# Optimization experiments

Hardware: AMD Instinct MI355X
Metric: run time of the kernel (lower is better)

Reference implementation:

```python
import jax, jax.numpy as jnp
import numpy as np

N_NODES = 10000
N_EDGES = 320000
IN_FEATS = 500
CONV_DIMS = [500, 256, 256]
FC_DIMS = [256, 128, 40]
BN_EPS = 1e-5


def setup_inputs() -> dict:
    key = jax.random.key(0)
    ks = jax.random.split(key, 16)
    inp = {
        "x": jax.random.normal(ks[0], (N_NODES, IN_FEATS), dtype=jnp.float32),
        "edge_index": jax.random.randint(ks[1], (2, N_EDGES), 0, N_NODES, dtype=jnp.int64),
    }
    # conv layer params: Linear W [in,out], b [out]; BatchNorm gamma/beta [out]
    ki = 2
    for li in range(len(CONV_DIMS) - 1):
        d_in, d_out = CONV_DIMS[li], CONV_DIMS[li + 1]
        s = 1.0 / np.sqrt(d_in)
        inp[f"conv_W{li}"] = jax.random.uniform(ks[ki], (d_in, d_out), jnp.float32, -s, s); ki += 1
        inp[f"conv_b{li}"] = jax.random.uniform(ks[ki], (d_out,), jnp.float32, -s, s); ki += 1
        inp[f"bn_g{li}"] = jnp.ones((d_out,), jnp.float32)
        inp[f"bn_b{li}"] = jnp.zeros((d_out,), jnp.float32)
    for li in range(len(FC_DIMS) - 1):
        d_in, d_out = FC_DIMS[li], FC_DIMS[li + 1]
        s = 1.0 / np.sqrt(d_in)
        inp[f"fc_W{li}"] = jax.random.uniform(ks[ki], (d_in, d_out), jnp.float32, -s, s); ki += 1
        inp[f"fc_b{li}"] = jax.random.uniform(ks[ki], (d_out,), jnp.float32, -s, s); ki += 1
    return inp


def _degree(edge_index, n, dtype):
    # Faithful to: A = eye(N); A[i,j] = 1 per edge (set semantics dedupes repeats).
    A = jnp.eye(n, dtype=dtype).at[edge_index[0], edge_index[1]].set(1.0)
    return A.sum(axis=1)  # deg_i = rowsum of A


def _batchnorm(h, g, b):
    # training-mode BatchNorm1d: batch stats, biased variance
    mean = h.mean(axis=0)
    var = h.var(axis=0)
    return (h - mean) * jax.lax.rsqrt(var + BN_EPS) * g + b


def reference(x, edge_index, conv_W0, conv_b0, bn_g0, bn_b0,
              conv_W1, conv_b1, bn_g1, bn_b1,
              fc_W0, fc_b0, fc_W1, fc_b1):
    n = x.shape[0]
    deg = _degree(edge_index, n, x.dtype)
    # D = sqrt(diag(deg)) is a diagonal matrix, so elementwise D*A*D = diag(deg);
    # mm(D*A*D, x) == deg[:, None] * x (exactly the original math).
    h = x
    for W, b, g, beta in ((conv_W0, conv_b0, bn_g0, bn_b0),
                          (conv_W1, conv_b1, bn_g1, bn_b1)):
        h = (deg[:, None] * h) @ W + b
        h = jax.nn.relu(h)
        h = _batchnorm(h, g, beta)
        # dropout: identity at inference
    for W, b in ((fc_W0, fc_b0), (fc_W1, fc_b1)):
        h = jax.nn.relu(h @ W + b)  # original appends ReLU after every fc, incl. last
    return h
```

## Files before the change

kernel.cpp:

```cpp
#include <hip/hip_runtime.h>

#define NN 10000
#define NE 320000
#define MP 10112
#define BN_EPS 1e-5f

#define NRANGE 64
#define BROWS 160
#define NBUCK 128
#define HBITS 5120
#define HWORDS 160
#define BCAP  4096
#define EPB   5000

typedef __attribute__((ext_vector_type(8))) short short8;
typedef __attribute__((ext_vector_type(4))) float f32x4;
typedef unsigned short u16;

__device__ __forceinline__ void split1(float v, u16& h, u16& l) {
    unsigned int u = __float_as_uint(v);
    h = (u16)(u >> 16);
    float hf = __uint_as_float(u & 0xFFFF0000u);
    l = (u16)(__float_as_uint(v - hf) >> 16);
}

__device__ __forceinline__ void gll16(const void* g, void* l) {
    __builtin_amdgcn_global_load_lds(
        (const __attribute__((address_space(1))) unsigned int*)g,
        (__attribute__((address_space(3))) unsigned int*)l, 16, 0, 0);
}

__device__ void splitW_dev(const float* __restrict__ W, int K, int N, int Kp, int Np,
                           u16* __restrict__ Wt, int bx, int by, char* smem) {
    float (*tile)[65] = (float(*)[65])smem;
    int t = threadIdx.x;
    int bk = bx * 64, bn = by * 64;
    #pragma unroll
    for (int p = 0; p < 4; ++p) {
        int kk = (t >> 4) + p * 16;
        int nc = (t & 15) * 4;
        int k = bk + kk;
        float4 v = {0.f, 0.f, 0.f, 0.f};
        if (k < K && bn + nc + 3 < N)
            v = *(const float4*)&W[(size_t)k * N + bn + nc];
        tile[kk][nc] = v.x; tile[kk][nc + 1] = v.y;
        tile[kk][nc + 2] = v.z; tile[kk][nc + 3] = v.w;
    }
    __syncthreads();
    int nn = t >> 2;
    int kk0 = (t & 3) * 16;
    u16 hs[16], ls[16];
    #pragma unroll
    for (int j = 0; j < 16; ++j) split1(tile[kk0 + j][nn], hs[j], ls[j]);
    size_t ob = (size_t)(bn + nn) * Kp + bk + kk0;
    size_t lo = (size_t)Np * Kp;
    *(short8*)&Wt[ob] = *(short8*)hs;
    *(short8*)&Wt[ob + 8] = *(short8*)&hs[8];
    *(short8*)&Wt[lo + ob] = *(short8*)ls;
    *(short8*)&Wt[lo + ob + 8] = *(short8*)&ls[8];
}

__device__ void xsplit_dev(const float* __restrict__ x, u16* __restrict__ xs, int gblk) {
    int t = threadIdx.x;
    int r0 = gblk * 16 + (t >> 4);
    int l = t & 15;
    u16* xlo = xs + (size_t)MP * 512;
    #pragma unroll
    for (int j = 0; j < 8; ++j) {
        int k = (l + j * 16) * 4;
        float vals[4] = {0.f, 0.f, 0.f, 0.f};
        if (r0 < NN && k < 500) {
            float4 v = *(const float4*)&x[(size_t)r0 * 500 + k];
            vals[0] = v.x; vals[1] = v.y; vals[2] = v.z; vals[3] = v.w;
        }
        ushort4 hs, ls;
        split1(vals[0], hs.x, ls.x); split1(vals[1], hs.y, ls.y);
        split1(vals[2], hs.z, ls.z); split1(vals[3], hs.w, ls.w);
        *(ushort4*)&xs[(size_t)r0 * 512 + k] = hs;
        *(ushort4*)&xlo[(size_t)r0 * 512 + k] = ls;
    }
}

__global__ __launch_bounds__(256)
void scatter_prep(const int* __restrict__ ei,
                  unsigned* __restrict__ bucketArr, unsigned* __restrict__ gcount,
                  const float* __restrict__ x,
                  const float* __restrict__ W0, const float* __restrict__ fW1,
                  u16* __restrict__ xs, u16* __restrict__ W0t, u16* __restrict__ fW1t) {
    __shared__ char smem[16704];
    __shared__ unsigned cnt[NBUCK], basep[NBUCK];
    int b = blockIdx.x;
    int t = threadIdx.x;
    if (b < 64) {
        if (t < NBUCK) cnt[t] = 0;
        __syncthreads();
        int base = b * EPB;
        unsigned myb[20], myk[20];
        #pragma unroll
        for (int k = 0; k < 20; ++k) {
            int el = t + k * 256;
            myb[k] = 0xFFFFFFFFu;
            if (el < EPB) {
                int e = base + el;
                unsigned i = (unsigned)ei[e], j = (unsigned)ei[NE + e];
                unsigned bk = (i / BROWS) * 2 + (j >= HBITS ? 1u : 0u);
                myb[k] = bk;
                myk[k] = (i << 14) | j;
                atomicAdd(&cnt[bk], 1u);
            }
        }
        __syncthreads();
        if (t < NBUCK) { basep[t] = atomicAdd(&gcount[t * 16], cnt[t]); cnt[t] = 0; }
        __syncthreads();
        #pragma unroll
        for (int k = 0; k < 20; ++k) {
            if (myb[k] != 0xFFFFFFFFu) {
                unsigned bk = myb[k];
                unsigned pos = basep[bk] + atomicAdd(&cnt[bk], 1u);
                if (pos < BCAP) bucketArr[(size_t)bk * BCAP + pos] = myk[k];
            }
        }
    } else if (b < 696) {
        xsplit_dev(x, xs, b - 64);
    } else if (b < 728) {
        int idx = b - 696;
        splitW_dev(W0, 500, 256, 512, 256, W0t, idx & 7, idx >> 3, smem);
    } else {
        splitW_dev(fW1, 128, 40, 128, 64, fW1t, b - 728, 0, smem);
    }
}

__global__ __launch_bounds__(256)
void bucket_degree(const unsigned* __restrict__ bucketArr,
                   const unsigned* __restrict__ gcount,
                   float* __restrict__ deg) {
    __shared__ unsigned lbm[BROWS * HWORDS];
    int b = blockIdx.x, t = threadIdx.x;
    int rr = b >> 1, h = b & 1;
    int row0 = rr * BROWS;
    {
        uint4* z = (uint4*)lbm;
        #pragma unroll
        for (int i = 0; i < 25; ++i) z[t + i * 256] = (uint4){0u, 0u, 0u, 0u};
    }
    __syncthreads();
    for (int r = t; r < BROWS; r += 256) {
        int i = row0 + r;
        if (i < NN && ((i >= HBITS) == (h == 1))) {
            int jj = i - h * HBITS;
            atomicOr(&lbm[r * HWORDS + (jj >> 5)], 1u << (jj & 31));
        }
    }
    unsigned n = gcount[b * 16];
    const unsigned* keys = bucketArr + (size_t)b * BCAP;
    for (unsigned k = t; k < n; k += 256) {
        unsigned key = keys[k];
        unsigned i = key >> 14, j = key & 0x3FFFu;
        unsigned r = i - row0;
        unsigned jj = j - h * HBITS;
        atomicOr(&lbm[r * HWORDS + (jj >> 5)], 1u << (jj & 31));
    }
    __syncthreads();
    #pragma unroll
    for (int pass = 0; pass < 3; ++pass) {
        int r = pass * 64 + (t >> 2), wl = t & 3;
        if (r >= BROWS) break;
        int i = row0 + r;
        int c = 0;
        const uint4* rp = (const uint4*)&lbm[r * HWORDS + wl * 40];
        #pragma unroll
        for (int m = 0; m < 10; ++m) {
            uint4 v = rp[m];
            c += __popc(v.x) + __popc(v.y) + __popc(v.z) + __popc(v.w);
        }
        c += __shfl_down(c, 1, 4);
        c += __shfl_down(c, 2, 4);
        if (wl == 0 && i < NN) atomicAdd(&deg[i], (float)c);
    }
}

__global__ __launch_bounds__(256, 4)
void conv0_gemm(const u16* __restrict__ Ahi, const u16* __restrict__ Alo,
                const u16* __restrict__ Bhi, const u16* __restrict__ Blo,
                const float* __restrict__ deg, const float* __restrict__ bias,
                float* __restrict__ stats,
                u16* __restrict__ Ohi, u16* __restrict__ Olo) {
    __shared__ char smem[32768];
    __shared__ float sdeg[64];
    const int Kp = 512, M = NN, No = 256;
    const int b = blockIdx.x;
    const int xcd = b & 7, g = b >> 3;
    const int bx = g & 3, by = (g >> 2) * 8 + xcd;
    if (by >= 158) return;
    const int t = threadIdx.x;
    const int lane = t & 63;
    const int w = t >> 6;
    const int q = lane >> 4;
    const int l16 = lane & 15;
    const int m7 = l16 & 7;
    const int row0 = by * 64;
    const int col0 = bx * 64;

    const u16* bases[4] = {Ahi, Alo, Bhi, Blo};
    const u16* srcs[8];
    unsigned dstoff[8];
    #pragma unroll
    for (int i = 0; i < 8; ++i) {
        int gi = w + i * 4;
        int reg = i >> 1;
        int j = gi & 7;
        int rb = (reg < 2) ? row0 : col0;
        int r = j * 8 + (lane >> 3);
        int c = (lane & 7) ^ (r & 7);
        srcs[i] = bases[reg] + (size_t)(rb + r) * Kp + c * 8;
        dstoff[i] = reg * 8192 + j * 1024;
    }

    f32x4 acc[4];
    #pragma unroll
    for (int s = 0; s < 4; ++s) acc[s] = (f32x4){0.f, 0.f, 0.f, 0.f};

    #pragma unroll
    for (int i = 0; i < 8; ++i) { gll16(srcs[i], smem + dstoff[i]); srcs[i] += 64; }

    if (t < 64) sdeg[t] = deg[row0 + t];

    for (int k0 = 0; k0 < Kp; k0 += 64) {
        __syncthreads();
        short8 ah[2], al[2], bh[2][4], bl[2][4];
        #pragma unroll
        for (int kc = 0; kc < 2; ++kc) {
            int aoff = (w * 16 + l16) * 128 + (((kc * 4 + q) ^ m7) * 16);
            ah[kc] = *(const short8*)(smem + aoff);
            al[kc] = *(const short8*)(smem + 8192 + aoff);
            #pragma unroll
            for (int s = 0; s < 4; ++s) {
                int boff = (s * 16 + l16) * 128 + (((kc * 4 + q) ^ m7) * 16);
                bh[kc][s] = *(const short8*)(smem + 16384 + boff);
                bl[kc][s] = *(const short8*)(smem + 24576 + boff);
            }
        }
        __syncthreads();
        if (k0 + 64 < Kp) {
            #pragma unroll
            for (int i = 0; i < 8; ++i) { gll16(srcs[i], smem + dstoff[i]); srcs[i] += 64; }
        }
        #pragma unroll
        for (int kc = 0; kc < 2; ++kc)
            #pragma unroll
            for (int s = 0; s < 4; ++s) {
                acc[s] = __builtin_amdgcn_mfma_f32_16x16x32_bf16(al[kc], bh[kc][s], acc[s], 0, 0, 0);
                acc[s] = __builtin_amdgcn_mfma_f32_16x16x32_bf16(ah[kc], bl[kc][s], acc[s], 0, 0, 0);
                acc[s] = __builtin_amdgcn_mfma_f32_16x16x32_bf16(ah[kc], bh[kc][s], acc[s], 0, 0, 0);
            }
    }

    int growb = row0 + w * 16 + q * 4;
    float dgv[4];
    #pragma unroll
    for (int r = 0; r < 4; ++r) {
        int grow = growb + r;
        dgv[r] = (grow < M) ? sdeg[grow - row0] : 0.f;
    }
    #pragma unroll
    for (int s = 0; s < 4; ++s) {
        int gc = col0 + s * 16 + l16;
        float bia = bias[gc];
        float s_sum = 0.f, ss_sum = 0.f;
        #pragma unroll
        for (int r = 0; r < 4; ++r) {
            int grow = growb + r;
            bool real = grow < M;
            float v = fmaxf(fmaf(dgv[r], acc[s][r], bia), 0.f);
            if (!real) v = 0.f;
            s_sum += v; ss_sum += v * v;
            float vo = v * dgv[r];
            u16 h, l; split1(vo, h, l);
            Ohi[(size_t)grow * No + gc] = h;
            Olo[(size_t)grow * No + gc] = l;
        }
        s_sum  += __shfl_xor(s_sum, 16);  s_sum  += __shfl_xor(s_sum, 32);
        ss_sum += __shfl_xor(ss_sum, 16); ss_sum += __shfl_xor(ss_sum, 32);
        if (lane < 16) {
            atomicAdd(&stats[gc], s_sum);
            atomicAdd(&stats[256 + gc], ss_sum);
        }
    }
}

__global__ __launch_bounds__(256, 4)
void conv1_fold(const u16* __restrict__ Ahi, const u16* __restrict__ Alo,
                const float* __restrict__ W1, const float* __restrict__ stats0,
                const float* __restrict__ g0, const float* __restrict__ bb0,
                const float* __restrict__ b1, const float* __restrict__ deg,
                float* __restrict__ stats1, u16* __restrict__ Ohi, u16* __restrict__ Olo) {
    __shared__ char smem[32768];
    __shared__ float scl[256], sh[256], cred[256], cvec[64];
    const int Kp = 256, M = NN, No = 256;
    const int b = blockIdx.x;
    const int xcd = b & 7, g = b >> 3;
    const int bx = g & 3, by = (g >> 2) * 8 + xcd;
    if (by >= 158) return;
    const int t = threadIdx.x;
    const int lane = t & 63;
    const int w = t >> 6;
    const int q = lane >> 4;
    const int l16 = lane & 15;
    const int m7 = l16 & 7;
    const int row0 = by * 64;
    const int col0 = bx * 64;

    const u16* srcs[4];
    unsigned dstoff[4];
    #pragma unroll
    for (int i = 0; i < 4; ++i) {
        int gi = w + i * 4;
        int plane = gi >> 3, j = gi & 7;
        int r = j * 8 + (lane >> 3);
        int c = (lane & 7) ^ (r & 7);
        srcs[i] = (plane ? Alo : Ahi) + (size_t)(row0 + r) * Kp + c * 8;
        dstoff[i] = plane * 8192 + j * 1024;
    }
    #pragma unroll
    for (int i = 0; i < 4; ++i) { gll16(srcs[i], smem + dstoff[i]); srcs[i] += 64; }

    {
        float mean = stats0[t] * (1.f / NN);
        float var = stats0[256 + t] * (1.f / NN) - mean * mean;
        float s = g0[t] * rsqrtf(var + BN_EPS);
        scl[t] = s;
        sh[t] = bb0[t] - mean * s;
    }
    __syncthreads();
    {
        float s = 0.f;
        int n = col0 + (t & 63);
        #pragma unroll 8
        for (int k = (t >> 6); k < 256; k += 4)
            s += sh[k] * W1[(size_t)k * 256 + n];
        cred[t] = s;
        __syncthreads();
        if (t < 64) cvec[t] = cred[t] + cred[t + 64] + cred[t + 128] + cred[t + 192];
    }
    const int bn = t & 63;
    const int kb = (t >> 6) * 16;
    const int ch0 = (t >> 6) * 2;
    float vals[16];
    {
        const float* wp = W1 + (size_t)kb * 256 + col0 + bn;
        #pragma unroll
        for (int i = 0; i < 16; ++i) vals[i] = wp[(size_t)i * 256] * scl[kb + i];
    }

    f32x4 acc[4];
    #pragma unroll
    for (int s = 0; s < 4; ++s) acc[s] = (f32x4){0.f, 0.f, 0.f, 0.f};

    for (int k0 = 0; k0 < Kp; k0 += 64) {
        {
            u16 hs[16], ls[16];
            #pragma unroll
            for (int i = 0; i < 16; ++i) split1(vals[i], hs[i], ls[i]);
            unsigned o0 = bn * 128 + ((ch0 ^ (bn & 7)) * 16);
            unsigned o1 = bn * 128 + (((ch0 + 1) ^ (bn & 7)) * 16);
            *(short8*)(smem + 16384 + o0) = *(short8*)&hs[0];
            *(short8*)(smem + 16384 + o1) = *(short8*)&hs[8];
            *(short8*)(smem + 24576 + o0) = *(short8*)&ls[0];
            *(short8*)(smem + 24576 + o1) = *(short8*)&ls[8];
        }
        __syncthreads();
        short8 ah[2], al[2], bh[2][4], bl[2][4];
        #pragma unroll
        for (int kc = 0; kc < 2; ++kc) {
            int aoff = (w * 16 + l16) * 128 + (((kc * 4 + q) ^ m7) * 16);
            ah[kc] = *(const short8*)(smem + aoff);
            al[kc] = *(const short8*)(smem + 8192 + aoff);
            #pragma unroll
            for (int s = 0; s < 4; ++s) {
                int boff = (s * 16 + l16) * 128 + (((kc * 4 + q) ^ m7) * 16);
                bh[kc][s] = *(const short8*)(smem + 16384 + boff);
                bl[kc][s] = *(const short8*)(smem + 24576 + boff);
            }
        }
        __syncthreads();
        if (k0 + 64 < Kp) {
            #pragma unroll
            for (int i = 0; i < 4; ++i) { gll16(srcs[i], smem + dstoff[i]); srcs[i] += 64; }
            const float* wp = W1 + (size_t)(k0 + 64 + kb) * 256 + col0 + bn;
            #pragma unroll
            for (int i = 0; i < 16; ++i) vals[i] = wp[(size_t)i * 256] * scl[k0 + 64 + kb + i];
        }
        #pragma unroll
        for (int kc = 0; kc < 2; ++kc)
            #pragma unroll
            for (int s = 0; s < 4; ++s) {
                acc[s] = __builtin_amdgcn_mfma_f32_16x16x32_bf16(al[kc], bh[kc][s], acc[s], 0, 0, 0);
                acc[s] = __builtin_amdgcn_mfma_f32_16x16x32_bf16(ah[kc], bl[kc][s], acc[s], 0, 0, 0);
                acc[s] = __builtin_amdgcn_mfma_f32_16x16x32_bf16(ah[kc], bh[kc][s], acc[s], 0, 0, 0);
            }
    }

    int growb = row0 + w * 16 + q * 4;
    float dgv[4];
    #pragma unroll
    for (int r = 0; r < 4; ++r) dgv[r] = (growb + r < M) ? deg[growb + r] : 0.f;
    #pragma unroll
    for (int s = 0; s < 4; ++s) {
        int gc = col0 + s * 16 + l16;
        float bia = b1[gc];
        float cv = cvec[s * 16 + l16];
        float s_sum = 0.f, ss_sum = 0.f;
        #pragma unroll
        for (int r = 0; r < 4; ++r) {
            int grow = growb + r;
            bool real = grow < M;
            float v = fmaxf(fmaf(dgv[r], cv, acc[s][r] + bia), 0.f);
            if (!real) v = 0.f;
            s_sum += v; ss_sum += v * v;
            u16 h, l; split1(v, h, l);
            Ohi[(size_t)grow * No + gc] = h;
            Olo[(size_t)grow * No + gc] = l;
        }
        s_sum  += __shfl_xor(s_sum, 16);  s_sum  += __shfl_xor(s_sum, 32);
        ss_sum += __shfl_xor(ss_sum, 16); ss_sum += __shfl_xor(ss_sum, 32);
        if (lane < 16) {
            atomicAdd(&stats1[gc], s_sum);
            atomicAdd(&stats1[256 + gc], ss_sum);
        }
    }
}

__global__ __launch_bounds__(256, 4)
void fc0_fold(const u16* __restrict__ Ahi, const u16* __restrict__ Alo,
              const float* __restrict__ fW0, const float* __restrict__ stats1,
              const float* __restrict__ g1, const float* __restrict__ bb1,
              const float* __restrict__ fb0,
              u16* __restrict__ Ohi, u16* __restrict__ Olo) {
    __shared__ char smem[32768];
    __shared__ float scl[256], sh[256], cred[256], biasf[64];
    const int Kp = 256, M = NN, No = 128;
    const int b = blockIdx.x;
    const int xcd = b & 7, g = b >> 3;
    const int bx = g & 1, by = (g >> 1) * 8 + xcd;
    if (by >= 158) return;
    const int t = threadIdx.x;
    const int lane = t & 63;
    const int w = t >> 6;
    const int q = lane >> 4;
    const int l16 = lane & 15;
    const int m7 = l16 & 7;
    const int row0 = by * 64;
    const int col0 = bx * 64;

    const u16* srcs[4];
    unsigned dstoff[4];
    #pragma unroll
    for (int i = 0; i < 4; ++i) {
        int gi = w + i * 4;
        int plane = gi >> 3, j = gi & 7;
        int r = j * 8 + (lane >> 3);
        int c = (lane & 7) ^ (r & 7);
        srcs[i] = (plane ? Alo : Ahi) + (size_t)(row0 + r) * Kp + c * 8;
        dstoff[i] = plane * 8192 + j * 1024;
    }
    #pragma unroll
    for (int i = 0; i < 4; ++i) { gll16(srcs[i], smem + dstoff[i]); srcs[i] += 64; }

    {
        float mean = stats1[t] * (1.f / NN);
        float var = stats1[256 + t] * (1.f / NN) - mean * mean;
        float s = g1[t] * rsqrtf(var + BN_EPS);
        scl[t] = s;
        sh[t] = bb1[t] - mean * s;
    }
    __syncthreads();
    {
        float s = 0.f;
        int n = col0 + (t & 63);
        #pragma unroll 8
        for (int k = (t >> 6); k < 256; k += 4)
            s += sh[k] * fW0[(size_t)k * 128 + n];
        cred[t] = s;
        __syncthreads();
        if (t < 64)
            biasf[t] = fb0[col0 + t] + cred[t] + cred[t + 64] + cred[t + 128] + cred[t + 192];
    }
    const int bn = t & 63;
    const int kb = (t >> 6) * 16;
    const int ch0 = (t >> 6) * 2;
    float vals[16];
    {
        const float* wp = fW0 + (size_t)kb * 128 + col0 + bn;
        #pragma unroll
        for (int i = 0; i < 16; ++i) vals[i] = wp[(size_t)i * 128] * scl[kb + i];
    }

    f32x4 acc[4];
    #pragma unroll
    for (int s = 0; s < 4; ++s) acc[s] = (f32x4){0.f, 0.f, 0.f, 0.f};

    for (int k0 = 0; k0 < Kp; k0 += 64) {
        {
            u16 hs[16], ls[16];
            #pragma unroll
            for (int i = 0; i < 16; ++i) split1(vals[i], hs[i], ls[i]);
            unsigned o0 = bn * 128 + ((ch0 ^ (bn & 7)) * 16);
            unsigned o1 = bn * 128 + (((ch0 + 1) ^ (bn & 7)) * 16);
            *(short8*)(smem + 16384 + o0) = *(short8*)&hs[0];
            *(short8*)(smem + 16384 + o1) = *(short8*)&hs[8];
            *(short8*)(smem + 24576 + o0) = *(short8*)&ls[0];
            *(short8*)(smem + 24576 + o1) = *(short8*)&ls[8];
        }
        __syncthreads();
        short8 ah[2], al[2], bh[2][4], bl[2][4];
        #pragma unroll
        for (int kc = 0; kc < 2; ++kc) {
            int aoff = (w * 16 + l16) * 128 + (((kc * 4 + q) ^ m7) * 16);
            ah[kc] = *(const short8*)(smem + aoff);
            al[kc] = *(const short8*)(smem + 8192 + aoff);
            #pragma unroll
            for (int s = 0; s < 4; ++s) {
                int boff = (s * 16 + l16) * 128 + (((kc * 4 + q) ^ m7) * 16);
                bh[kc][s] = *(const short8*)(smem + 16384 + boff);
                bl[kc][s] = *(const short8*)(smem + 24576 + boff);
            }
        }
        __syncthreads();
        if (k0 + 64 < Kp) {
            #pragma unroll
            for (int i = 0; i < 4; ++i) { gll16(srcs[i], smem + dstoff[i]); srcs[i] += 64; }
            const float* wp = fW0 + (size_t)(k0 + 64 + kb) * 128 + col0 + bn;
            #pragma unroll
            for (int i = 0; i < 16; ++i) vals[i] = wp[(size_t)i * 128] * scl[k0 + 64 + kb + i];
        }
        #pragma unroll
        for (int kc = 0; kc < 2; ++kc)
            #pragma unroll
            for (int s = 0; s < 4; ++s) {
                acc[s] = __builtin_amdgcn_mfma_f32_16x16x32_bf16(al[kc], bh[kc][s], acc[s], 0, 0, 0);
                acc[s] = __builtin_amdgcn_mfma_f32_16x16x32_bf16(ah[kc], bl[kc][s], acc[s], 0, 0, 0);
                acc[s] = __builtin_amdgcn_mfma_f32_16x16x32_bf16(ah[kc], bh[kc][s], acc[s], 0, 0, 0);
            }
    }

    int growb = row0 + w * 16 + q * 4;
    #pragma unroll
    for (int s = 0; s < 4; ++s) {
        int gc = col0 + s * 16 + l16;
        float bia = biasf[s * 16 + l16];
        #pragma unroll
        for (int r = 0; r < 4; ++r) {
            int grow = growb + r;
            float v = fmaxf(acc[s][r] + bia, 0.f);
            if (grow >= M) v = 0.f;
            u16 h, l; split1(v, h, l);
            Ohi[(size_t)grow * No + gc] = h;
            Olo[(size_t)grow * No + gc] = l;
        }
    }
}

__global__ __launch_bounds__(256, 3)
void fc1_gemm(const u16* __restrict__ Ahi, const u16* __restrict__ Alo,
              const u16* __restrict__ Bhi, const u16* __restrict__ Blo,
              const float* __restrict__ bias, float* __restrict__ out) {
    __shared__ char smem[32768];
    const int Kp = 128, M = NN, N = 40, No = 40;
    const int t = threadIdx.x;
    const int lane = t & 63;
    const int w = t >> 6;
    const int q = lane >> 4;
    const int l16 = lane & 15;
    const int m7 = l16 & 7;
    const int row0 = blockIdx.x * 64;
    const int col0 = 0;

    const u16* bases[4] = {Ahi, Alo, Bhi, Blo};
    const u16* srcs[8];
    unsigned dstoff[8];
    #pragma unroll
    for (int i = 0; i < 8; ++i) {
        int gi = w + i * 4;
        int reg = i >> 1;
        int j = gi & 7;
        int rb = (reg < 2) ? row0 : col0;
        int r = j * 8 + (lane >> 3);
        int c = (lane & 7) ^ (r & 7);
        srcs[i] = bases[reg] + (size_t)(rb + r) * Kp + c * 8;
        dstoff[i] = reg * 8192 + j * 1024;
    }

    f32x4 acc[4];
    #pragma unroll
    for (int s = 0; s < 4; ++s) acc[s] = (f32x4){0.f, 0.f, 0.f, 0.f};

    #pragma unroll
    for (int i = 0; i < 8; ++i) { gll16(srcs[i], smem + dstoff[i]); srcs[i] += 64; }

    for (int k0 = 0; k0 < Kp; k0 += 64) {
        __syncthreads();
        short8 ah[2], al[2], bh[2][4], bl[2][4];
        #pragma unroll
        for (int kc = 0; kc < 2; ++kc) {
            int aoff = (w * 16 + l16) * 128 + (((kc * 4 + q) ^ m7) * 16);
            ah[kc] = *(const short8*)(smem + aoff);
            al[kc] = *(const short8*)(smem + 8192 + aoff);
            #pragma unroll
            for (int s = 0; s < 4; ++s) {
                int boff = (s * 16 + l16) * 128 + (((kc * 4 + q) ^ m7) * 16);
                bh[kc][s] = *(const short8*)(smem + 16384 + boff);
                bl[kc][s] = *(const short8*)(smem + 24576 + boff);
            }
        }
        __syncthreads();
        if (k0 + 64 < Kp) {
            #pragma unroll
            for (int i = 0; i < 8; ++i) { gll16(srcs[i], smem + dstoff[i]); srcs[i] += 64; }
        }
        #pragma unroll
        for (int kc = 0; kc < 2; ++kc)
            #pragma unroll
            for (int s = 0; s < 4; ++s) {
                acc[s] = __builtin_amdgcn_mfma_f32_16x16x32_bf16(al[kc], bh[kc][s], acc[s], 0, 0, 0);
                acc[s] = __builtin_amdgcn_mfma_f32_16x16x32_bf16(ah[kc], bl[kc][s], acc[s], 0, 0, 0);
                acc[s] = __builtin_amdgcn_mfma_f32_16x16x32_bf16(ah[kc], bh[kc][s], acc[s], 0, 0, 0);
            }
    }

    int growb = row0 + w * 16 + q * 4;
    #pragma unroll
    for (int s = 0; s < 4; ++s) {
        int gc = col0 + s * 16 + l16;
        if (gc >= N) continue;
        float bia = bias[gc];
        #pragma unroll
        for (int r = 0; r < 4; ++r) {
            int grow = growb + r;
            if (grow < M)
                out[(size_t)grow * No + gc] = fmaxf(acc[s][r] + bia, 0.f);
        }
    }
}


extern "C" void kernel_launch(void* const* d_in, const int* in_sizes, int n_in,
                              void* d_out, int out_size, void* d_ws, size_t ws_size,
                              hipStream_t stream) {
    const float* x   = (const float*)d_in[0];
    const int*   ei  = (const int*)d_in[1];
    const float* W0  = (const float*)d_in[2];
    const float* b0  = (const float*)d_in[3];
    const float* g0  = (const float*)d_in[4];
    const float* bb0 = (const float*)d_in[5];
    const float* W1  = (const float*)d_in[6];
    const float* b1  = (const float*)d_in[7];
    const float* g1  = (const float*)d_in[8];
    const float* bb1 = (const float*)d_in[9];
    const float* fW0 = (const float*)d_in[10];
    const float* fb0 = (const float*)d_in[11];
    const float* fW1 = (const float*)d_in[12];
    const float* fb1 = (const float*)d_in[13];
    float* out = (float*)d_out;

    char* ws = (char*)d_ws;
    auto carve = [&](size_t bytes) { char* q = ws; ws += (bytes + 255) & ~(size_t)255; return q; };

    const size_t ZERO_BYTES = 4096 + 8192 + (size_t)MP * 4;
    char* region0 = carve(ZERO_BYTES);
    float* stats = (float*)region0;
    unsigned* gcount = (unsigned*)(region0 + 4096);
    float* deg   = (float*)(region0 + 4096 + 8192);

    unsigned* bucketArr = (unsigned*)carve((size_t)NBUCK * BCAP * 4);
    u16* xs     = (u16*)carve((size_t)2 * MP * 512 * 2);
    u16* W0t    = (u16*)carve((size_t)2 * 256 * 512 * 2);
    u16* fW1t   = (u16*)carve((size_t)2 * 64 * 128 * 2);
    u16* H1     = (u16*)carve((size_t)2 * MP * 256 * 2);
    u16* H2     = (u16*)carve((size_t)2 * MP * 256 * 2);
    u16* H3     = (u16*)carve((size_t)2 * MP * 128 * 2);

    dim3 blk(256);

    hipMemsetAsync(region0, 0, ZERO_BYTES, stream);
    scatter_prep<<<730, blk, 0, stream>>>(ei, bucketArr, gcount, x, W0, fW1, xs, W0t, fW1t);
    bucket_degree<<<NBUCK, blk, 0, stream>>>(bucketArr, gcount, deg);
    conv0_gemm<<<640, blk, 0, stream>>>(
        xs, xs + (size_t)MP * 512, W0t, W0t + 256 * 512,
        deg, b0, stats, H1, H1 + (size_t)MP * 256);
    conv1_fold<<<640, blk, 0, stream>>>(
        H1, H1 + (size_t)MP * 256, W1, stats, g0, bb0, b1, deg,
        stats + 512, H2, H2 + (size_t)MP * 256);
    fc0_fold<<<320, blk, 0, stream>>>(
        H2, H2 + (size_t)MP * 256, fW0, stats + 512, g1, bb1, fb0,
        H3, H3 + (size_t)MP * 128);
    fc1_gemm<<<158, blk, 0, stream>>>(
        H3, H3 + (size_t)MP * 128, fW1t, fW1t + 64 * 128, fb1, out);
}
```

Before: 179.9 us.

## Fuse x bf16 split into conv0 GEMM and drop memset via per-block sub-buckets

The separate pre-pass that split x into hi/lo bf16 planes in global memory is removed. conv0_gemm now loads fp32 x directly, splits it in registers and writes the planes into shared memory each K step, which avoids writing and re-reading a 20 MB intermediate. Edge bucketing now uses fixed per-source-block sub-buckets with local counters, and degree halves are written rather than atomically added. Stats are zeroed inside scatter_prep, so the hipMemsetAsync is dropped. In exchange, the GEMM does more ALU work and issues direct global loads per K step, and each per-block sub-bucket is capped at SUBCAP=128 entries, beyond which edges would be dropped silently.

```diff
diff --git a/kernel.cpp b/kernel.cpp
--- a/kernel.cpp
+++ b/kernel.cpp
@@ -10,7 +10,7 @@
 #define NBUCK 128
 #define HBITS 5120
 #define HWORDS 160
-#define BCAP  4096
+#define SUBCAP 128
 #define EPB   5000
 
 typedef __attribute__((ext_vector_type(8))) short short8;
@@ -60,80 +60,50 @@
     *(short8*)&Wt[lo + ob + 8] = *(short8*)&ls[8];
 }
 
-__device__ void xsplit_dev(const float* __restrict__ x, u16* __restrict__ xs, int gblk) {
-    int t = threadIdx.x;
-    int r0 = gblk * 16 + (t >> 4);
-    int l = t & 15;
-    u16* xlo = xs + (size_t)MP * 512;
-    #pragma unroll
-    for (int j = 0; j < 8; ++j) {
-        int k = (l + j * 16) * 4;
-        float vals[4] = {0.f, 0.f, 0.f, 0.f};
-        if (r0 < NN && k < 500) {
-            float4 v = *(const float4*)&x[(size_t)r0 * 500 + k];
-            vals[0] = v.x; vals[1] = v.y; vals[2] = v.z; vals[3] = v.w;
-        }
-        ushort4 hs, ls;
-        split1(vals[0], hs.x, ls.x); split1(vals[1], hs.y, ls.y);
-        split1(vals[2], hs.z, ls.z); split1(vals[3], hs.w, ls.w);
-        *(ushort4*)&xs[(size_t)r0 * 512 + k] = hs;
-        *(ushort4*)&xlo[(size_t)r0 * 512 + k] = ls;
-    }
-}
-
 __global__ __launch_bounds__(256)
 void scatter_prep(const int* __restrict__ ei,
-                  unsigned* __restrict__ bucketArr, unsigned* __restrict__ gcount,
-                  const float* __restrict__ x,
+                  unsigned* __restrict__ bucketArr, unsigned* __restrict__ cnts,
+                  float* __restrict__ stats,
                   const float* __restrict__ W0, const float* __restrict__ fW1,
-                  u16* __restrict__ xs, u16* __restrict__ W0t, u16* __restrict__ fW1t) {
+                  u16* __restrict__ W0t, u16* __restrict__ fW1t) {
     __shared__ char smem[16704];
-    __shared__ unsigned cnt[NBUCK], basep[NBUCK];
+    __shared__ unsigned cnt[NBUCK];
     int b = blockIdx.x;
     int t = threadIdx.x;
     if (b < 64) {
         if (t < NBUCK) cnt[t] = 0;
         __syncthreads();
         int base = b * EPB;
-        unsigned myb[20], myk[20];
         #pragma unroll
         for (int k = 0; k < 20; ++k) {
             int el = t + k * 256;
-            myb[k] = 0xFFFFFFFFu;
             if (el < EPB) {
                 int e = base + el;
                 unsigned i = (unsigned)ei[e], j = (unsigned)ei[NE + e];
                 unsigned bk = (i / BROWS) * 2 + (j >= HBITS ? 1u : 0u);
-                myb[k] = bk;
-                myk[k] = (i << 14) | j;
-                atomicAdd(&cnt[bk], 1u);
-            }
-        }
-        __syncthreads();
-        if (t < NBUCK) { basep[t] = atomicAdd(&gcount[t * 16], cnt[t]); cnt[t] = 0; }
-        __syncthreads();
-        #pragma unroll
-        for (int k = 0; k < 20; ++k) {
-            if (myb[k] != 0xFFFFFFFFu) {
-                unsigned bk = myb[k];
-                unsigned pos = basep[bk] + atomicAdd(&cnt[bk], 1u);
-                if (pos < BCAP) bucketArr[(size_t)bk * BCAP + pos] = myk[k];
-            }
-        }
-    } else if (b < 696) {
-        xsplit_dev(x, xs, b - 64);
-    } else if (b < 728) {
-        int idx = b - 696;
+                unsigned key = (i << 14) | j;
+                unsigned pos = atomicAdd(&cnt[bk], 1u);
+                if (pos < SUBCAP)
+                    bucketArr[((size_t)bk << 13) + ((unsigned)b << 7) + pos] = key;
+            }
+        }
+        __syncthreads();
+        if (t < NBUCK) cnts[(t << 6) + b] = min(cnt[t], (unsigned)SUBCAP);
+    } else if (b < 96) {
+        int idx = b - 64;
         splitW_dev(W0, 500, 256, 512, 256, W0t, idx & 7, idx >> 3, smem);
     } else {
-        splitW_dev(fW1, 128, 40, 128, 64, fW1t, b - 728, 0, smem);
+        int base = (b - 96) * 512;
+        stats[base + t] = 0.f;
+        stats[base + 256 + t] = 0.f;
+        splitW_dev(fW1, 128, 40, 128, 64, fW1t, b - 96, 0, smem);
     }
 }
 
 __global__ __launch_bounds__(256)
 void bucket_degree(const unsigned* __restrict__ bucketArr,
-                   const unsigned* __restrict__ gcount,
-                   float* __restrict__ deg) {
+                   const unsigned* __restrict__ cnts,
+                   float* __restrict__ degh) {
     __shared__ unsigned lbm[BROWS * HWORDS];
     int b = blockIdx.x, t = threadIdx.x;
     int rr = b >> 1, h = b & 1;
@@ -151,14 +121,17 @@
             atomicOr(&lbm[r * HWORDS + (jj >> 5)], 1u << (jj & 31));
         }
     }
-    unsigned n = gcount[b * 16];
-    const unsigned* keys = bucketArr + (size_t)b * BCAP;
-    for (unsigned k = t; k < n; k += 256) {
-        unsigned key = keys[k];
-        unsigned i = key >> 14, j = key & 0x3FFFu;
-        unsigned r = i - row0;
-        unsigned jj = j - h * HBITS;
-        atomicOr(&lbm[r * HWORDS + (jj >> 5)], 1u << (jj & 31));
+    {
+        int sb = t >> 2, kl = t & 3;
+        unsigned n = cnts[(b << 6) + sb];
+        const unsigned* keys = bucketArr + ((size_t)b << 13) + ((unsigned)sb << 7);
+        for (unsigned k = kl; k < n; k += 4) {
+            unsigned key = keys[k];
+            unsigned i = key >> 14, j = key & 0x3FFFu;
+            unsigned r = i - row0;
+            unsigned jj = j - h * HBITS;
+            atomicOr(&lbm[r * HWORDS + (jj >> 5)], 1u << (jj & 31));
+        }
     }
     __syncthreads();
     #pragma unroll
@@ -175,14 +148,14 @@
         }
         c += __shfl_down(c, 1, 4);
         c += __shfl_down(c, 2, 4);
-        if (wl == 0 && i < NN) atomicAdd(&deg[i], (float)c);
+        if (wl == 0 && i < MP) degh[h * MP + i] = (float)c;
     }
 }
 
 __global__ __launch_bounds__(256, 4)
-void conv0_gemm(const u16* __restrict__ Ahi, const u16* __restrict__ Alo,
+void conv0_gemm(const float* __restrict__ x,
                 const u16* __restrict__ Bhi, const u16* __restrict__ Blo,
-                const float* __restrict__ deg, const float* __restrict__ bias,
+                const float* __restrict__ degh, const float* __restrict__ bias,
                 float* __restrict__ stats,
                 u16* __restrict__ Ohi, u16* __restrict__ Olo) {
     __shared__ char smem[32768];
@@ -201,31 +174,55 @@
     const int row0 = by * 64;
     const int col0 = bx * 64;
 
-    const u16* bases[4] = {Ahi, Alo, Bhi, Blo};
-    const u16* srcs[8];
-    unsigned dstoff[8];
-    #pragma unroll
-    for (int i = 0; i < 8; ++i) {
-        int gi = w + i * 4;
-        int reg = i >> 1;
-        int j = gi & 7;
-        int rb = (reg < 2) ? row0 : col0;
+    const u16* srcs[4];
+    unsigned dstoff[4];
+    #pragma unroll
+    for (int i = 0; i < 4; ++i) {
+        int j = w + (i & 1) * 4;
+        int plane = i >> 1;
         int r = j * 8 + (lane >> 3);
         int c = (lane & 7) ^ (r & 7);
-        srcs[i] = bases[reg] + (size_t)(rb + r) * Kp + c * 8;
-        dstoff[i] = reg * 8192 + j * 1024;
-    }
+        srcs[i] = (plane ? Blo : Bhi) + (size_t)(col0 + r) * Kp + c * 8;
+        dstoff[i] = 16384 + plane * 8192 + j * 1024;
+    }
+    #pragma unroll
+    for (int i = 0; i < 4; ++i) { gll16(srcs[i], smem + dstoff[i]); srcs[i] += 64; }
+
+    const int rn = t & 63;
+    const int c4 = t >> 6;
+    const int ch0 = c4 * 2;
+    float vals[16];
+    {
+        int row = row0 + rn;
+        const float* xp = x + (size_t)row * 500 + c4 * 16;
+        #pragma unroll
+        for (int m = 0; m < 4; ++m) {
+            float4 v = {0.f, 0.f, 0.f, 0.f};
+            if (row < NN && (c4 * 16 + m * 4) < 500)
+                v = *(const float4*)(xp + m * 4);
+            vals[m * 4 + 0] = v.x; vals[m * 4 + 1] = v.y;
+            vals[m * 4 + 2] = v.z; vals[m * 4 + 3] = v.w;
+        }
+    }
+
+    if (t < 64) sdeg[t] = degh[row0 + t] + degh[MP + row0 + t];
 
     f32x4 acc[4];
     #pragma unroll
     for (int s = 0; s < 4; ++s) acc[s] = (f32x4){0.f, 0.f, 0.f, 0.f};
 
-    #pragma unroll
-    for (int i = 0; i < 8; ++i) { gll16(srcs[i], smem + dstoff[i]); srcs[i] += 64; }
-
-    if (t < 64) sdeg[t] = deg[row0 + t];
-
     for (int k0 = 0; k0 < Kp; k0 += 64) {
+        {
+            u16 hs[16], ls[16];
+            #pragma unroll
+            for (int i2 = 0; i2 < 16; ++i2) split1(vals[i2], hs[i2], ls[i2]);
+            unsigned o0 = rn * 128 + ((ch0 ^ (rn & 7)) * 16);
+            unsigned o1 = rn * 128 + (((ch0 + 1) ^ (rn & 7)) * 16);
+            *(short8*)(smem + o0) = *(short8*)&hs[0];
+            *(short8*)(smem + o1) = *(short8*)&hs[8];
+            *(short8*)(smem + 8192 + o0) = *(short8*)&ls[0];
+            *(short8*)(smem + 8192 + o1) = *(short8*)&ls[8];
+        }
         __syncthreads();
         short8 ah[2], al[2], bh[2][4], bl[2][4];
         #pragma unroll
@@ -243,7 +240,17 @@
         __syncthreads();
         if (k0 + 64 < Kp) {
             #pragma unroll
-            for (int i = 0; i < 8; ++i) { gll16(srcs[i], smem + dstoff[i]); srcs[i] += 64; }
+            for (int i = 0; i < 4; ++i) { gll16(srcs[i], smem + dstoff[i]); srcs[i] += 64; }
+            int row = row0 + rn;
+            const float* xp = x + (size_t)row * 500 + k0 + 64 + c4 * 16;
+            #pragma unroll
+            for (int m = 0; m < 4; ++m) {
+                float4 v = {0.f, 0.f, 0.f, 0.f};
+                if (row < NN && (k0 + 64 + c4 * 16 + m * 4) < 500)
+                    v = *(const float4*)(xp + m * 4);
+                vals[m * 4 + 0] = v.x; vals[m * 4 + 1] = v.y;
+                vals[m * 4 + 2] = v.z; vals[m * 4 + 3] = v.w;
+            }
         }
         #pragma unroll
         for (int kc = 0; kc < 2; ++kc)
@@ -292,7 +299,7 @@
 void conv1_fold(const u16* __restrict__ Ahi, const u16* __restrict__ Alo,
                 const float* __restrict__ W1, const float* __restrict__ stats0,
                 const float* __restrict__ g0, const float* __restrict__ bb0,
-                const float* __restrict__ b1, const float* __restrict__ deg,
+                const float* __restrict__ b1, const float* __restrict__ degh,
                 float* __restrict__ stats1, u16* __restrict__ Ohi, u16* __restrict__ Olo) {
     __shared__ char smem[32768];
     __shared__ float scl[256], sh[256], cred[256], cvec[64];
@@ -403,7 +410,10 @@
     int growb = row0 + w * 16 + q * 4;
     float dgv[4];
     #pragma unroll
-    for (int r = 0; r < 4; ++r) dgv[r] = (growb + r < M) ? deg[growb + r] : 0.f;
+    for (int r = 0; r < 4; ++r) {
+        int grow = growb + r;
+        dgv[r] = (grow < M) ? (degh[grow] + degh[MP + grow]) : 0.f;
+    }
     #pragma unroll
     for (int s = 0; s < 4; ++s) {
         int gc = col0 + s * 16 + l16;
@@ -665,14 +675,10 @@
     char* ws = (char*)d_ws;
     auto carve = [&](size_t bytes) { char* q = ws; ws += (bytes + 255) & ~(size_t)255; return q; };
 
-    const size_t ZERO_BYTES = 4096 + 8192 + (size_t)MP * 4;
-    char* region0 = carve(ZERO_BYTES);
-    float* stats = (float*)region0;
-    unsigned* gcount = (unsigned*)(region0 + 4096);
-    float* deg   = (float*)(region0 + 4096 + 8192);
-
-    unsigned* bucketArr = (unsigned*)carve((size_t)NBUCK * BCAP * 4);
-    u16* xs     = (u16*)carve((size_t)2 * MP * 512 * 2);
+    float* stats = (float*)carve(4096);
+    unsigned* cnts = (unsigned*)carve((size_t)NBUCK * 64 * 4);
+    float* degh = (float*)carve((size_t)2 * MP * 4);
+    unsigned* bucketArr = (unsigned*)carve((size_t)NBUCK * 64 * SUBCAP * 4);
     u16* W0t    = (u16*)carve((size_t)2 * 256 * 512 * 2);
     u16* fW1t   = (u16*)carve((size_t)2 * 64 * 128 * 2);
     u16* H1     = (u16*)carve((size_t)2 * MP * 256 * 2);
@@ -681,14 +687,12 @@
 
     dim3 blk(256);
 
-    hipMemsetAsync(region0, 0, ZERO_BYTES, stream);
-    scatter_prep<<<730, blk, 0, stream>>>(ei, bucketArr, gcount, x, W0, fW1, xs, W0t, fW1t);
-    bucket_degree<<<NBUCK, blk, 0, stream>>>(bucketArr, gcount, deg);
+    scatter_prep<<<98, blk, 0, stream>>>(ei, bucketArr, cnts, stats, W0, fW1, W0t, fW1t);
+    bucket_degree<<<NBUCK, blk, 0, stream>>>(bucketArr, cnts, degh);
     conv0_gemm<<<640, blk, 0, stream>>>(
-        xs, xs + (size_t)MP * 512, W0t, W0t + 256 * 512,
-        deg, b0, stats, H1, H1 + (size_t)MP * 256);
+        x, W0t, W0t + 256 * 512, degh, b0, stats, H1, H1 + (size_t)MP * 256);
     conv1_fold<<<640, blk, 0, stream>>>(
-        H1, H1 + (size_t)MP * 256, W1, stats, g0, bb0, b1, deg,
+        H1, H1 + (size_t)MP * 256, W1, stats, g0, bb0, b1, degh,
         stats + 512, H2, H2 + (size_t)MP * 256);
     fc0_fold<<<320, blk, 0, stream>>>(
         H2, H2 + (size_t)MP * 256, fW0, stats + 512, g1, bb1, fb0,
```

New measurement: 188.4 us. 4.7% more time.
